# Kernel tuning notes

Hardware: AMD Instinct MI355X
Metric: run time of the kernel (lower is better)

## Reference

```python
import jax, jax.numpy as jnp
import numpy as np

NODE_DIM = 256
HID = 128        # out_channels per head
HEADS = 4
NLAYERS = 2
OUT_DIM = 128
LM, LT = 30, 50
N = LM + LT       # 80 nodes per duplex graph
F = HID * HEADS   # 512
B = 1024
LN_EPS = 1e-5

def _build_edges():
    off = LM
    ms = np.arange(LM - 1); md = ms + 1
    ts = off + np.arange(LT - 1); td = ts + 1
    s1 = np.concatenate([ms, md, ts, td]); d1 = np.concatenate([md, ms, td, ts])
    ms2 = np.arange(LM - 2); md2 = ms2 + 2
    ts2 = off + np.arange(LT - 2); td2 = ts2 + 2
    s2 = np.concatenate([ms2, md2, ts2, td2]); d2 = np.concatenate([md2, ms2, td2, ts2])
    src = np.concatenate([s1, s2]).astype(np.int32)
    dst = np.concatenate([d1, d2]).astype(np.int32)
    etype = np.concatenate([np.zeros(len(s1), np.int32), np.full(len(s2), 2, np.int32)])
    return src, dst, etype

_SRC0, _DST0, _ETYPE0 = _build_edges()
E0 = len(_SRC0)                      # 308 real edges (backbone + proximity)
SRC = jnp.concatenate([jnp.asarray(_SRC0), jnp.arange(N, dtype=jnp.int32)])  # + self loops
DST = jnp.concatenate([jnp.asarray(_DST0), jnp.arange(N, dtype=jnp.int32)])
DST_BASE = jnp.asarray(_DST0)
ETYPE = jnp.asarray(_ETYPE0)

def _ln(x, g, b):
    mu = x.mean(-1, keepdims=True)
    var = ((x - mu) ** 2).mean(-1, keepdims=True)
    return (x - mu) * jax.lax.rsqrt(var + LN_EPS) * g + b

def setup_inputs() -> dict:
    key = jax.random.key(0)
    ks = jax.random.split(key, 24)
    r = lambda k, shape, fan: jax.random.normal(k, shape, jnp.float32) / np.sqrt(fan)
    inp = {
        'mirna_enc': jax.random.normal(ks[0], (B, LM, NODE_DIM), jnp.float32),
        'target_enc': jax.random.normal(ks[1], (B, LT, NODE_DIM), jnp.float32),
        'node_type_emb': r(ks[2], (2, NODE_DIM), NODE_DIM),
        'edge_type_emb': r(ks[3], (3, HEADS), HEADS),
        'in_W': r(ks[4], (NODE_DIM, F), NODE_DIM), 'in_b': jnp.zeros((F,)),
        'in_ln_g': jnp.ones((F,)), 'in_ln_b': jnp.zeros((F,)),
        'gat_Wl': r(ks[5], (NLAYERS, F, F), F), 'gat_bl': jnp.zeros((NLAYERS, F)),
        'gat_Wr': r(ks[6], (NLAYERS, F, F), F), 'gat_br': jnp.zeros((NLAYERS, F)),
        'gat_We': r(ks[7], (NLAYERS, HEADS, F), HEADS),
        'gat_att': r(ks[8], (NLAYERS, HEADS, HID), HID),
        'gat_bo': jnp.zeros((NLAYERS, F)),
        'ln_g': jnp.ones((NLAYERS, F)), 'ln_b': jnp.zeros((NLAYERS, F)),
        'out_W': r(ks[9], (2 * F, OUT_DIM), 2 * F), 'out_b': jnp.zeros((OUT_DIM,)),
        'out_ln_g': jnp.ones((OUT_DIM,)), 'out_ln_b': jnp.zeros((OUT_DIM,)),
    }
    return inp

def reference(mirna_enc, target_enc, node_type_emb, edge_type_emb, in_W, in_b,
              in_ln_g, in_ln_b, gat_Wl, gat_bl, gat_Wr, gat_br, gat_We, gat_att,
              gat_bo, ln_g, ln_b, out_W, out_b, out_ln_g, out_ln_b):
    bsz = mirna_enc.shape[0]
    x = jnp.concatenate([mirna_enc + node_type_emb[0], target_enc + node_type_emb[1]], axis=1)  # [B,N,256]
    x = jax.nn.gelu(_ln(x @ in_W + in_b, in_ln_g, in_ln_b), approximate=False)  # [B,N,F]
    # edge attributes; self-loop attr = per-dst mean of incoming edge attrs (PyG fill_value='mean')
    base = edge_type_emb[ETYPE]  # [E0, HEADS]
    cnt = jax.ops.segment_sum(jnp.ones((E0, 1), base.dtype), DST_BASE, num_segments=N)
    sl = jax.ops.segment_sum(base, DST_BASE, num_segments=N) / jnp.maximum(cnt, 1.0)
    e_attr = jnp.concatenate([base, sl], axis=0)  # [E, HEADS]
    for i in range(NLAYERS):
        ee = (e_attr @ gat_We[i]).reshape(-1, HEADS, HID)                 # [E,H,C]
        xl = (x @ gat_Wl[i] + gat_bl[i]).reshape(bsz, N, HEADS, HID)
        xr = (x @ gat_Wr[i] + gat_br[i]).reshape(bsz, N, HEADS, HID)
        att_i = gat_att[i]
        def one_graph(xl_b, xr_b):
            msg = xl_b[SRC] + xr_b[DST] + ee                              # [E,H,C]
            a = jnp.einsum('ehc,hc->eh', jax.nn.leaky_relu(msg, 0.2), att_i)
            amax = jax.ops.segment_max(a, DST, num_segments=N)            # every node has a self loop
            ex = jnp.exp(a - amax[DST])
            den = jax.ops.segment_sum(ex, DST, num_segments=N)
            alpha = ex / den[DST]                                         # [E,H]
            out = jax.ops.segment_sum(alpha[:, :, None] * xl_b[SRC], DST, num_segments=N)
            return out.reshape(N, F)
        h = jax.vmap(one_graph)(xl, xr) + gat_bo[i]
        x = _ln(h + x, ln_g[i], ln_b[i])
        if i < NLAYERS - 1:
            x = jax.nn.gelu(x, approximate=False)
    pooled = jnp.concatenate([x.mean(axis=1), x.max(axis=1)], axis=-1)    # [B, 2F]
    return jax.nn.gelu(_ln(pooled @ out_W + out_b, out_ln_g, out_ln_b), approximate=False)
```

## Files before the change

kernel.cpp:

```cpp
#include <hip/hip_runtime.h>
#include <hip/hip_bf16.h>

typedef unsigned short u16;
typedef unsigned int u32;
typedef __attribute__((ext_vector_type(8))) short bf16x8;
typedef __attribute__((ext_vector_type(4))) float f32x4;

#define NB   1024
#define LMI  30
#define LTG  50
#define NN   80
#define ROWS (NB*NN)
#define FF   512
#define HH   4
#define CC   128

__device__ __forceinline__ u16 f2b(float f) {
    u32 u = __float_as_uint(f);
    u32 r = (u + 0x7FFFu + ((u >> 16) & 1u)) >> 16;
    return (u16)r;
}
__device__ __forceinline__ float b2f(u16 h) {
    return __uint_as_float(((u32)h) << 16);
}
__device__ __forceinline__ float gelu_f(float v) {
    return 0.5f * v * (1.0f + erff(v * 0.70710678118654752440f));
}
__device__ __forceinline__ void gload_lds16(const void* g, void* l) {
    __builtin_amdgcn_global_load_lds(
        (__attribute__((address_space(1))) void*)(uintptr_t)g,
        (__attribute__((address_space(3))) void*)(uintptr_t)l,
        16, 0, 0);
}

#define X_OFF     0ULL
#define XLR_OFF   83886080ULL
#define INWT_OFF  251658240ULL
#define WLRT_OFF  (INWT_OFF + 262144ULL)
#define BIAS_OFF  (WLRT_OFF + 2097152ULL)
#define EER_OFF   (BIAS_OFF + 8192ULL)
#define EES_OFF   (EER_OFF + 8192ULL)

__global__ __launch_bounds__(256)
void prep_misc(const float* __restrict__ in_W, const float* __restrict__ gat_Wl,
               const float* __restrict__ gat_bl, const float* __restrict__ gat_Wr,
               const float* __restrict__ gat_br, const float* __restrict__ gat_We,
               const float* __restrict__ eemb,
               u16* __restrict__ inWt, u16* __restrict__ Wlrt,
               float* __restrict__ biaslr, float* __restrict__ eereal,
               float* __restrict__ eeself)
{
    int idx = blockIdx.x * 256 + threadIdx.x;
    if (idx < 131072) {
        int n = idx >> 8, k = idx & 255;
        inWt[idx] = f2b(in_W[k * 512 + n]);
        return;
    }
    idx -= 131072;
    if (idx < 1048576) {
        int l = idx >> 19; int r = idx & 524287; int n = r >> 9, k = r & 511;
        float v = (n < 512) ? gat_Wl[(size_t)l * 262144 + (size_t)k * 512 + n]
                            : gat_Wr[(size_t)l * 262144 + (size_t)k * 512 + (n - 512)];
        Wlrt[idx] = f2b(v);
        return;
    }
    idx -= 1048576;
    if (idx < 2048) {
        int l = idx >> 10, n = idx & 1023;
        biaslr[idx] = (n < 512) ? gat_bl[l * 512 + n] : gat_br[l * 512 + (n - 512)];
        return;
    }
    idx -= 2048;
    if (idx < 2048) {
        int l = idx >> 10; int r = idx & 1023; int t = r >> 9, f = r & 511;
        int et = t ? 2 : 0;
        float v = 0.f;
        #pragma unroll
        for (int h = 0; h < 4; ++h)
            v += eemb[et * 4 + h] * gat_We[l * 2048 + h * 512 + f];
        eereal[idx] = v;
        return;
    }
    idx -= 2048;
    if (idx < 81920) {
        int l = idx / 40960; int r = idx % 40960; int n = r >> 9, f = r & 511;
        int LL = (n < LMI) ? LMI : LTG;
        int p  = (n < LMI) ? n : (n - LMI);
        float c1 = (float)((p >= 1) + (p <= LL - 2));
        float c2 = (float)((p >= 2) + (p <= LL - 3));
        float ic = 1.0f / (c1 + c2);
        float v = 0.f;
        #pragma unroll
        for (int h = 0; h < 4; ++h) {
            float attr = (c1 * eemb[0 * 4 + h] + c2 * eemb[2 * 4 + h]) * ic;
            v += attr * gat_We[l * 2048 + h * 512 + f];
        }
        eeself[idx] = v;
        return;
    }
}

__global__ __launch_bounds__(64)
void prep_xin(const float* __restrict__ mirna, const float* __restrict__ target,
              const float* __restrict__ nte, u16* __restrict__ xin)
{
    int bid = blockIdx.x;
    int b = bid / NN, n = bid % NN;
    int t = threadIdx.x;
    const float* src; const float* tv;
    if (n < LMI) { src = mirna + ((size_t)b * LMI + n) * 256; tv = nte; }
    else         { src = target + ((size_t)b * LTG + (n - LMI)) * 256; tv = nte + 256; }
    float4 v = *(const float4*)(src + t * 4);
    float4 e = *(const float4*)(tv + t * 4);
    u32 p0 = (u32)f2b(v.x + e.x) | ((u32)f2b(v.y + e.y) << 16);
    u32 p1 = (u32)f2b(v.z + e.z) | ((u32)f2b(v.w + e.w) << 16);
    *(uint2*)(xin + (size_t)bid * 256 + t * 4) = make_uint2(p0, p1);
}

template<int N, int K>
__global__ __launch_bounds__(512, 2)
void gemm_nt_bias(const u16* __restrict__ A, const u16* __restrict__ Bt,
                  const float* __restrict__ bias, u16* __restrict__ Cout)
{
    __shared__ __align__(16) u16 sm[4][2][8192];
    const int tid = threadIdx.x;
    const int w = tid >> 6, l = tid & 63;
    constexpr int ncb = N / 256;

    const int per = gridDim.x >> 3;
    const int nid = (blockIdx.x & 7) * per + (blockIdx.x >> 3);
    const int row0 = (nid / ncb) * 256;
    const int col0 = (nid % ncb) * 256;
    const int wr = w >> 2, wc = w & 3;

    const int srow = l >> 2;
    const int kperm = ((l & 3) ^ ((l >> 3) & 3)) * 8;
    const u16* Ag0 = A  + (size_t)(row0 +       w * 16 + srow) * K + kperm;
    const u16* Ag1 = A  + (size_t)(row0 + 128 + w * 16 + srow) * K + kperm;
    const u16* Bg0 = Bt + (size_t)(col0 +       w * 16 + srow) * K + kperm;
    const u16* Bg1 = Bt + (size_t)(col0 + 128 + w * 16 + srow) * K + kperm;
    const int lc0 = w * 512, lc1 = (8 + w) * 512;

#define STAGE_A(buf, t) do { \
        gload_lds16(Ag0 + (size_t)(t) * 32, &sm[buf][0][lc0]); \
        gload_lds16(Ag1 + (size_t)(t) * 32, &sm[buf][0][lc1]); } while (0)
#define STAGE_B(buf, t) do { \
        gload_lds16(Bg0 + (size_t)(t) * 32, &sm[buf][1][lc0]); \
        gload_lds16(Bg1 + (size_t)(t) * 32, &sm[buf][1][lc1]); } while (0)

    f32x4 acc[8][4];
    #pragma unroll
    for (int r = 0; r < 8; ++r)
        #pragma unroll
        for (int f = 0; f < 4; ++f)
            acc[r][f] = (f32x4){0.f, 0.f, 0.f, 0.f};

    constexpr int nsteps = K >> 5;
    STAGE_A(0, 0); STAGE_B(0, 0);
    STAGE_A(1, 1); STAGE_B(1, 1);

    const int pslot = ((l >> 4) ^ (((l & 15) >> 1) & 3)) * 8;
    const int abase = wr * 8 * 512 + (l & 15) * 32 + pslot;
    const int bbase = wc * 4 * 512 + (l & 15) * 32 + pslot;

    #pragma unroll
    for (int t = 0; t < nsteps; ++t) {
        const int buf = t & 3;
        if (t + 1 < nsteps) {
            asm volatile("s_waitcnt vmcnt(4)" ::: "memory");
        } else {
            asm volatile("s_waitcnt vmcnt(0)" ::: "memory");
        }
        __builtin_amdgcn_s_barrier();
        asm volatile("" ::: "memory");

        bf16x8 bfr[4], af[4];
        #pragma unroll
        for (int fc = 0; fc < 4; ++fc)
            bfr[fc] = *(const bf16x8*)&sm[buf][1][bbase + fc * 512];
        #pragma unroll
        for (int fr = 0; fr < 4; ++fr)
            af[fr] = *(const bf16x8*)&sm[buf][0][abase + fr * 512];
        if (t + 2 < nsteps) STAGE_A((t + 2) & 3, t + 2);
        __builtin_amdgcn_s_setprio(1);
        #pragma unroll
        for (int fr = 0; fr < 4; ++fr)
            #pragma unroll
            for (int fc = 0; fc < 4; ++fc)
                acc[fr][fc] = __builtin_amdgcn_mfma_f32_16x16x32_bf16(bfr[fc], af[fr], acc[fr][fc], 0, 0, 0);
        __builtin_amdgcn_s_setprio(0);
        asm volatile("" ::: "memory");
        __builtin_amdgcn_s_barrier();
        asm volatile("" ::: "memory");

        #pragma unroll
        for (int fr = 0; fr < 4; ++fr)
            af[fr] = *(const bf16x8*)&sm[buf][0][abase + (4 + fr) * 512];
        if (t + 2 < nsteps) STAGE_B((t + 2) & 3, t + 2);
        __builtin_amdgcn_s_setprio(1);
        #pragma unroll
        for (int fr = 0; fr < 4; ++fr)
            #pragma unroll
            for (int fc = 0; fc < 4; ++fc)
                acc[4 + fr][fc] = __builtin_amdgcn_mfma_f32_16x16x32_bf16(bfr[fc], af[fr], acc[4 + fr][fc], 0, 0, 0);
        __builtin_amdgcn_s_setprio(0);
        asm volatile("" ::: "memory");
    }
#undef STAGE_A
#undef STAGE_B

    #pragma unroll
    for (int ar = 0; ar < 8; ++ar) {
        int grow = row0 + wr * 128 + ar * 16 + (l & 15);
        #pragma unroll
        for (int fc = 0; fc < 4; ++fc) {
            int n0 = col0 + wc * 64 + fc * 16 + (l >> 4) * 4;
            float4 bv = *(const float4*)(bias + n0);
            u32 lo = (u32)f2b(acc[ar][fc][0] + bv.x) | ((u32)f2b(acc[ar][fc][1] + bv.y) << 16);
            u32 hi = (u32)f2b(acc[ar][fc][2] + bv.z) | ((u32)f2b(acc[ar][fc][3] + bv.w) << 16);
            *(uint2*)&Cout[(size_t)grow * N + n0] = make_uint2(lo, hi);
        }
    }
}

__global__ __launch_bounds__(256)
void ln_gelu_rows(u16* __restrict__ x, const float* __restrict__ g, const float* __restrict__ b)
{
    int w = threadIdx.x >> 6, l = threadIdx.x & 63;
    size_t row = (size_t)blockIdx.x * 4 + w;
    u16* rp = x + row * FF + l * 8;
    bf16x8 v = *(const bf16x8*)rp;
    float y[8]; float s = 0.f, q = 0.f;
    #pragma unroll
    for (int j = 0; j < 8; ++j) { y[j] = b2f((u16)v[j]); s += y[j]; q += y[j] * y[j]; }
    #pragma unroll
    for (int st = 32; st; st >>= 1) { s += __shfl_xor(s, st, 64); q += __shfl_xor(q, st, 64); }
    float mu = s * (1.0f / 512.0f);
    float var = q * (1.0f / 512.0f) - mu * mu;
    float rs = rsqrtf(var + 1e-5f);
    float4 g0 = *(const float4*)(g + l * 8), g1 = *(const float4*)(g + l * 8 + 4);
    float4 b0 = *(const float4*)(b + l * 8), b1 = *(const float4*)(b + l * 8 + 4);
    float gv[8] = {g0.x, g0.y, g0.z, g0.w, g1.x, g1.y, g1.z, g1.w};
    float bv[8] = {b0.x, b0.y, b0.z, b0.w, b1.x, b1.y, b1.z, b1.w};
    bf16x8 o;
    #pragma unroll
    for (int j = 0; j < 8; ++j) {
        float z = (y[j] - mu) * rs * gv[j] + bv[j];
        o[j] = (short)f2b(gelu_f(z));
    }
    *(bf16x8*)rp = o;
}

__global__ __launch_bounds__(256)
void gat_layer(u16* __restrict__ x, const u16* __restrict__ xlr,
               const float* __restrict__ att, const float* __restrict__ eereal,
               const float* __restrict__ eeself, const float* __restrict__ bo,
               const float* __restrict__ g, const float* __restrict__ bta,
               int apply_gelu)
{
    int tid = threadIdx.x;
    int h = tid >> 6, l = tid & 63;
    int s = l >> 4, t = l & 15;
    int row = blockIdx.x * 4 + s;
    int n = row % NN;
    int lo = (n < LMI) ? 0 : LMI;
    int hi = (n < LMI) ? (LMI - 1) : (NN - 1);
    int c = h * CC + t * 8;

    bf16x8 xrv = *(const bf16x8*)(xlr + (size_t)row * 1024 + 512 + c);
    float xr[8], atv[8];
    #pragma unroll
    for (int j = 0; j < 8; ++j) xr[j] = b2f((u16)xrv[j]);
    {
        float4 a0 = *(const float4*)(att + c), a1 = *(const float4*)(att + c + 4);
        atv[0]=a0.x; atv[1]=a0.y; atv[2]=a0.z; atv[3]=a0.w;
        atv[4]=a1.x; atv[5]=a1.y; atv[6]=a1.z; atv[7]=a1.w;
    }

    bf16x8 vsave[5];
    float p5[5];
    float amax = -1e30f;
    #pragma unroll
    for (int i = 0; i < 5; ++i) {
        int d = i - 2;
        int src = n + d;
        bool ok = (src >= lo) && (src <= hi);
        int dd = ok ? d : 0;
        bf16x8 vv = *(const bf16x8*)(xlr + (size_t)(row + dd) * 1024 + c);
        vsave[i] = vv;
        const float* ee = (i == 2) ? (eeself + (size_t)n * 512 + c)
                        : ((i == 1 || i == 3) ? (eereal + c) : (eereal + 512 + c));
        float4 e0 = *(const float4*)ee, e1 = *(const float4*)(ee + 4);
        float eez[8] = {e0.x, e0.y, e0.z, e0.w, e1.x, e1.y, e1.z, e1.w};
        float p = 0.f;
        #pragma unroll
        for (int j = 0; j < 8; ++j) {
            float m = b2f((u16)vv[j]) + xr[j] + eez[j];
            m = m > 0.f ? m : 0.2f * m;
            p += m * atv[j];
        }
        p += __shfl_xor(p, 1, 64);
        p += __shfl_xor(p, 2, 64);
        p += __shfl_xor(p, 4, 64);
        p += __shfl_xor(p, 8, 64);
        p = ok ? p : -1e30f;
        p5[i] = p;
        amax = fmaxf(amax, p);
    }
    float den = 0.f;
    float o[8] = {0.f,0.f,0.f,0.f,0.f,0.f,0.f,0.f};
    #pragma unroll
    for (int i = 0; i < 5; ++i) {
        float ex = __expf(p5[i] - amax);
        den += ex;
        #pragma unroll
        for (int j = 0; j < 8; ++j) o[j] += ex * b2f((u16)vsave[i][j]);
    }
    float inv = 1.0f / den;

    u16* xrow = x + (size_t)row * FF + c;
    bf16x8 xv = *(const bf16x8*)xrow;
    float bov[8];
    {
        float4 b0 = *(const float4*)(bo + c), b1 = *(const float4*)(bo + c + 4);
        bov[0]=b0.x; bov[1]=b0.y; bov[2]=b0.z; bov[3]=b0.w;
        bov[4]=b1.x; bov[5]=b1.y; bov[6]=b1.z; bov[7]=b1.w;
    }
    float y[8]; float sum = 0.f, sq = 0.f;
    #pragma unroll
    for (int j = 0; j < 8; ++j) {
        y[j] = o[j] * inv + bov[j] + b2f((u16)xv[j]);
        sum += y[j]; sq += y[j] * y[j];
    }
    sum += __shfl_xor(sum, 1, 64); sq += __shfl_xor(sq, 1, 64);
    sum += __shfl_xor(sum, 2, 64); sq += __shfl_xor(sq, 2, 64);
    sum += __shfl_xor(sum, 4, 64); sq += __shfl_xor(sq, 4, 64);
    sum += __shfl_xor(sum, 8, 64); sq += __shfl_xor(sq, 8, 64);

    __shared__ float ssum[4][4], ssq[4][4];
    if (t == 0) { ssum[h][s] = sum; ssq[h][s] = sq; }
    __syncthreads();
    float tot = ssum[0][s] + ssum[1][s] + ssum[2][s] + ssum[3][s];
    float tq  = ssq[0][s] + ssq[1][s] + ssq[2][s] + ssq[3][s];
    float mu = tot * (1.0f / 512.0f);
    float var = tq * (1.0f / 512.0f) - mu * mu;
    float rs = rsqrtf(var + 1e-5f);

    float gv[8], btv[8];
    {
        float4 g0 = *(const float4*)(g + c), g1 = *(const float4*)(g + c + 4);
        float4 t0 = *(const float4*)(bta + c), t1 = *(const float4*)(bta + c + 4);
        gv[0]=g0.x; gv[1]=g0.y; gv[2]=g0.z; gv[3]=g0.w;
        gv[4]=g1.x; gv[5]=g1.y; gv[6]=g1.z; gv[7]=g1.w;
        btv[0]=t0.x; btv[1]=t0.y; btv[2]=t0.z; btv[3]=t0.w;
        btv[4]=t1.x; btv[5]=t1.y; btv[6]=t1.z; btv[7]=t1.w;
    }
    bf16x8 ov;
    #pragma unroll
    for (int j = 0; j < 8; ++j) {
        float z = (y[j] - mu) * rs * gv[j] + btv[j];
        if (apply_gelu) z = gelu_f(z);
        ov[j] = (short)f2b(z);
    }
    *(bf16x8*)xrow = ov;
}

__global__ __launch_bounds__(512)
void pool_kernel(const u16* __restrict__ x, u16* __restrict__ pooled)
{
    int b = blockIdx.x;
    int f = threadIdx.x;
    const u16* base = x + (size_t)b * NN * FF + f;
    float s = 0.f, mx = -1e30f;
    #pragma unroll 4
    for (int n = 0; n < NN; ++n) {
        float v = b2f(base[(size_t)n * FF]);
        s += v; mx = fmaxf(mx, v);
    }
    pooled[(size_t)b * 1024 + f]       = f2b(s * (1.0f / 80.0f));
    pooled[(size_t)b * 1024 + 512 + f] = f2b(mx);
}

__global__ __launch_bounds__(128)
void out_head(const u16* __restrict__ pooled, const float* __restrict__ W,
              const float* __restrict__ bia, const float* __restrict__ g,
              const float* __restrict__ bt, float* __restrict__ out)
{
    int b = blockIdx.x;
    int j = threadIdx.x;
    __shared__ float prow[1024];
    for (int i = j; i < 1024; i += 128) prow[i] = b2f(pooled[(size_t)b * 1024 + i]);
    __syncthreads();
    float acc = 0.f;
    #pragma unroll 8
    for (int k = 0; k < 1024; ++k) acc += prow[k] * W[k * 128 + j];
    acc += bia[j];
    float s = acc, q = acc * acc;
    #pragma unroll
    for (int st = 32; st; st >>= 1) { s += __shfl_xor(s, st, 64); q += __shfl_xor(q, st, 64); }
    __shared__ float ps[2], pq[2];
    int w = j >> 6;
    if ((j & 63) == 0) { ps[w] = s; pq[w] = q; }
    __syncthreads();
    float tot = ps[0] + ps[1], tq = pq[0] + pq[1];
    float mu = tot * (1.0f / 128.0f);
    float var = tq * (1.0f / 128.0f) - mu * mu;
    float rs = rsqrtf(var + 1e-5f);
    float z = (acc - mu) * rs * g[j] + bt[j];
    out[(size_t)b * 128 + j] = gelu_f(z);
}

extern "C" void kernel_launch(void* const* d_in, const int* in_sizes, int n_in,
                              void* d_out, int out_size, void* d_ws, size_t ws_size,
                              hipStream_t stream)
{
    (void)in_sizes; (void)n_in; (void)out_size; (void)ws_size;
    const float* mirna    = (const float*)d_in[0];
    const float* target   = (const float*)d_in[1];
    const float* nte      = (const float*)d_in[2];
    const float* eemb     = (const float*)d_in[3];
    const float* in_W     = (const float*)d_in[4];
    const float* in_b     = (const float*)d_in[5];
    const float* in_ln_g  = (const float*)d_in[6];
    const float* in_ln_b  = (const float*)d_in[7];
    const float* gat_Wl   = (const float*)d_in[8];
    const float* gat_bl   = (const float*)d_in[9];
    const float* gat_Wr   = (const float*)d_in[10];
    const float* gat_br   = (const float*)d_in[11];
    const float* gat_We   = (const float*)d_in[12];
    const float* gat_att  = (const float*)d_in[13];
    const float* gat_bo   = (const float*)d_in[14];
    const float* ln_g     = (const float*)d_in[15];
    const float* ln_b     = (const float*)d_in[16];
    const float* out_W    = (const float*)d_in[17];
    const float* out_b    = (const float*)d_in[18];
    const float* out_ln_g = (const float*)d_in[19];
    const float* out_ln_b = (const float*)d_in[20];

    char* ws = (char*)d_ws;
    u16*   x      = (u16*)(ws + X_OFF);
    u16*   xlr    = (u16*)(ws + XLR_OFF);
    u16*   xin    = xlr;
    u16*   pooled = xlr;
    u16*   inWt   = (u16*)(ws + INWT_OFF);
    u16*   Wlrt   = (u16*)(ws + WLRT_OFF);
    float* biaslr = (float*)(ws + BIAS_OFF);
    float* eereal = (float*)(ws + EER_OFF);
    float* eeself = (float*)(ws + EES_OFF);

    prep_misc<<<4944, 256, 0, stream>>>(in_W, gat_Wl, gat_bl, gat_Wr, gat_br, gat_We, eemb,
                                        inWt, Wlrt, biaslr, eereal, eeself);
    prep_xin<<<ROWS, 64, 0, stream>>>(mirna, target, nte, xin);

    gemm_nt_bias<512, 256><<<(ROWS / 256) * 2, 512, 0, stream>>>(xin, inWt, in_b, x);
    ln_gelu_rows<<<ROWS / 4, 256, 0, stream>>>(x, in_ln_g, in_ln_b);

    for (int l = 0; l < 2; ++l) {
        gemm_nt_bias<1024, 512><<<(ROWS / 256) * 4, 512, 0, stream>>>(
            x, Wlrt + (size_t)l * 524288, biaslr + l * 1024, xlr);
        gat_layer<<<ROWS / 4, 256, 0, stream>>>(x, xlr,
                                                gat_att + l * 512,
                                                eereal + l * 1024,
                                                eeself + (size_t)l * 40960,
                                                gat_bo + l * 512,
                                                ln_g + l * 512, ln_b + l * 512,
                                                (l == 0) ? 1 : 0);
    }

    pool_kernel<<<NB, 512, 0, stream>>>(x, pooled);
    out_head<<<NB, 128, 0, stream>>>(pooled, out_W, out_b, out_ln_g, out_ln_b, (float*)d_out);
}
```

Measured before the change: 565.9 us.

## Restructure GEMM mainloop to double-buffered K=64 tiles with quadrant-split MFMA phases

Switches the bf16 GEMM from a 4-deep ring of K=32 stages to a 2-buffer scheme with K=64 tiles, using a new XOR swizzle for the LDS layout. Each iteration now waits for all outstanding loads, issues the next tile's prefetch, and computes the 256x256 output in four quadrant phases separated by barriers. The aim is fewer loop iterations and barriers per unit of K and larger global loads per stage. The cost is a full vmcnt(0) wait each iteration, which shortens the prefetch distance, plus several extra barriers. The new register fragment layout also changes register pressure.

```diff
diff --git a/kernel.cpp b/kernel.cpp
--- a/kernel.cpp
+++ b/kernel.cpp
@@ -122,10 +122,11 @@
 void gemm_nt_bias(const u16* __restrict__ A, const u16* __restrict__ Bt,
                   const float* __restrict__ bias, u16* __restrict__ Cout)
 {
-    __shared__ __align__(16) u16 sm[4][2][8192];
+    __shared__ __align__(16) u16 sm[2][2][16384];
     const int tid = threadIdx.x;
     const int w = tid >> 6, l = tid & 63;
     constexpr int ncb = N / 256;
+    constexpr int KT = K / 64;
 
     const int per = gridDim.x >> 3;
     const int nid = (blockIdx.x & 7) * per + (blockIdx.x >> 3);
@@ -133,20 +134,24 @@
     const int col0 = (nid % ncb) * 256;
     const int wr = w >> 2, wc = w & 3;
 
-    const int srow = l >> 2;
-    const int kperm = ((l & 3) ^ ((l >> 3) & 3)) * 8;
-    const u16* Ag0 = A  + (size_t)(row0 +       w * 16 + srow) * K + kperm;
-    const u16* Ag1 = A  + (size_t)(row0 + 128 + w * 16 + srow) * K + kperm;
-    const u16* Bg0 = Bt + (size_t)(col0 +       w * 16 + srow) * K + kperm;
-    const u16* Bg1 = Bt + (size_t)(col0 + 128 + w * 16 + srow) * K + kperm;
-    const int lc0 = w * 512, lc1 = (8 + w) * 512;
-
-#define STAGE_A(buf, t) do { \
-        gload_lds16(Ag0 + (size_t)(t) * 32, &sm[buf][0][lc0]); \
-        gload_lds16(Ag1 + (size_t)(t) * 32, &sm[buf][0][lc1]); } while (0)
-#define STAGE_B(buf, t) do { \
-        gload_lds16(Bg0 + (size_t)(t) * 32, &sm[buf][1][lc0]); \
-        gload_lds16(Bg1 + (size_t)(t) * 32, &sm[buf][1][lc1]); } while (0)
+    const int srow = w * 8 + (l >> 3);
+    const int sks  = ((l & 7) ^ (l >> 3)) * 8;
+    const u16* Abase = A  + (size_t)(row0 + srow) * K + sks;
+    const u16* Bbase = Bt + (size_t)(col0 + srow) * K + sks;
+    const int ldst = w * 512;
+
+#define STAGE_KT(buf, kt) do {                                          \
+        const u16* _a = Abase + (size_t)(kt) * 64;                      \
+        const u16* _b = Bbase + (size_t)(kt) * 64;                      \
+        gload_lds16(_a,                   &sm[buf][0][ldst]);           \
+        gload_lds16(_a + (size_t)64  * K, &sm[buf][0][4096  + ldst]);   \
+        gload_lds16(_a + (size_t)128 * K, &sm[buf][0][8192  + ldst]);   \
+        gload_lds16(_a + (size_t)192 * K, &sm[buf][0][12288 + ldst]);   \
+        gload_lds16(_b,                   &sm[buf][1][ldst]);           \
+        gload_lds16(_b + (size_t)64  * K, &sm[buf][1][4096  + ldst]);   \
+        gload_lds16(_b + (size_t)128 * K, &sm[buf][1][8192  + ldst]);   \
+        gload_lds16(_b + (size_t)192 * K, &sm[buf][1][12288 + ldst]);   \
+    } while (0)
 
     f32x4 acc[8][4];
     #pragma unroll
@@ -155,66 +160,96 @@
         for (int f = 0; f < 4; ++f)
             acc[r][f] = (f32x4){0.f, 0.f, 0.f, 0.f};
 
-    constexpr int nsteps = K >> 5;
-    STAGE_A(0, 0); STAGE_B(0, 0);
-    STAGE_A(1, 1); STAGE_B(1, 1);
-
-    const int pslot = ((l >> 4) ^ (((l & 15) >> 1) & 3)) * 8;
-    const int abase = wr * 8 * 512 + (l & 15) * 32 + pslot;
-    const int bbase = wc * 4 * 512 + (l & 15) * 32 + pslot;
-
-    #pragma unroll
-    for (int t = 0; t < nsteps; ++t) {
-        const int buf = t & 3;
-        if (t + 1 < nsteps) {
-            asm volatile("s_waitcnt vmcnt(4)" ::: "memory");
-        } else {
-            asm volatile("s_waitcnt vmcnt(0)" ::: "memory");
-        }
-        __builtin_amdgcn_s_barrier();
-        asm volatile("" ::: "memory");
-
-        bf16x8 bfr[4], af[4];
-        #pragma unroll
-        for (int fc = 0; fc < 4; ++fc)
-            bfr[fc] = *(const bf16x8*)&sm[buf][1][bbase + fc * 512];
-        #pragma unroll
-        for (int fr = 0; fr < 4; ++fr)
-            af[fr] = *(const bf16x8*)&sm[buf][0][abase + fr * 512];
-        if (t + 2 < nsteps) STAGE_A((t + 2) & 3, t + 2);
+    const int ll = l & 15, lh = l >> 4;
+    const int x0 = ((lh)     ^ (ll & 7)) * 8;
+    const int x1 = ((4 + lh) ^ (ll & 7)) * 8;
+    const int aB = wr * 8192 + ll * 64;
+    const int bB = (wc >> 1) * 8192 + ((wc & 1) * 64 + ll) * 64;
+
+    STAGE_KT(0, 0);
+
+    #pragma unroll
+    for (int kt = 0; kt < KT; ++kt) {
+        const int cur = kt & 1;
+        asm volatile("s_waitcnt vmcnt(0)" ::: "memory");
+        __builtin_amdgcn_s_barrier();
+
+        bf16x8 a0[4][2], a1[4][2], b0[2][2], b1[2][2];
+        #pragma unroll
+        for (int fr = 0; fr < 4; ++fr) {
+            a0[fr][0] = *(const bf16x8*)&sm[cur][0][aB + fr * 1024 + x0];
+            a0[fr][1] = *(const bf16x8*)&sm[cur][0][aB + fr * 1024 + x1];
+        }
+        #pragma unroll
+        for (int fc = 0; fc < 2; ++fc) {
+            b0[fc][0] = *(const bf16x8*)&sm[cur][1][bB + fc * 1024 + x0];
+            b0[fc][1] = *(const bf16x8*)&sm[cur][1][bB + fc * 1024 + x1];
+        }
+        if (kt + 1 < KT) STAGE_KT(cur ^ 1, kt + 1);
+        __builtin_amdgcn_s_barrier();
         __builtin_amdgcn_s_setprio(1);
         #pragma unroll
         for (int fr = 0; fr < 4; ++fr)
             #pragma unroll
-            for (int fc = 0; fc < 4; ++fc)
-                acc[fr][fc] = __builtin_amdgcn_mfma_f32_16x16x32_bf16(bfr[fc], af[fr], acc[fr][fc], 0, 0, 0);
+            for (int fc = 0; fc < 2; ++fc)
+                #pragma unroll
+                for (int kk = 0; kk < 2; ++kk)
+                    acc[fr][fc] = __builtin_amdgcn_mfma_f32_16x16x32_bf16(b0[fc][kk], a0[fr][kk], acc[fr][fc], 0, 0, 0);
         __builtin_amdgcn_s_setprio(0);
-        asm volatile("" ::: "memory");
-        __builtin_amdgcn_s_barrier();
-        asm volatile("" ::: "memory");
-
-        #pragma unroll
-        for (int fr = 0; fr < 4; ++fr)
-            af[fr] = *(const bf16x8*)&sm[buf][0][abase + (4 + fr) * 512];
-        if (t + 2 < nsteps) STAGE_B((t + 2) & 3, t + 2);
+        __builtin_amdgcn_s_barrier();
+
+        #pragma unroll
+        for (int fc = 0; fc < 2; ++fc) {
+            b1[fc][0] = *(const bf16x8*)&sm[cur][1][bB + (2 + fc) * 1024 + x0];
+            b1[fc][1] = *(const bf16x8*)&sm[cur][1][bB + (2 + fc) * 1024 + x1];
+        }
+        __builtin_amdgcn_s_barrier();
         __builtin_amdgcn_s_setprio(1);
         #pragma unroll
         for (int fr = 0; fr < 4; ++fr)
             #pragma unroll
-            for (int fc = 0; fc < 4; ++fc)
-                acc[4 + fr][fc] = __builtin_amdgcn_mfma_f32_16x16x32_bf16(bfr[fc], af[fr], acc[4 + fr][fc], 0, 0, 0);
+            for (int fc = 0; fc < 2; ++fc)
+                #pragma unroll
+                for (int kk = 0; kk < 2; ++kk)
+                    acc[fr][2 + fc] = __builtin_amdgcn_mfma_f32_16x16x32_bf16(b1[fc][kk], a0[fr][kk], acc[fr][2 + fc], 0, 0, 0);
         __builtin_amdgcn_s_setprio(0);
-        asm volatile("" ::: "memory");
-    }
-#undef STAGE_A
-#undef STAGE_B
+        __builtin_amdgcn_s_barrier();
+
+        #pragma unroll
+        for (int fr = 0; fr < 4; ++fr) {
+            a1[fr][0] = *(const bf16x8*)&sm[cur][0][aB + (4 + fr) * 1024 + x0];
+            a1[fr][1] = *(const bf16x8*)&sm[cur][0][aB + (4 + fr) * 1024 + x1];
+        }
+        __builtin_amdgcn_s_barrier();
+        __builtin_amdgcn_s_setprio(1);
+        #pragma unroll
+        for (int fr = 0; fr < 4; ++fr)
+            #pragma unroll
+            for (int fc = 0; fc < 2; ++fc)
+                #pragma unroll
+                for (int kk = 0; kk < 2; ++kk)
+                    acc[4 + fr][fc] = __builtin_amdgcn_mfma_f32_16x16x32_bf16(b0[fc][kk], a1[fr][kk], acc[4 + fr][fc], 0, 0, 0);
+        __builtin_amdgcn_s_setprio(0);
+        __builtin_amdgcn_s_barrier();
+
+        __builtin_amdgcn_s_setprio(1);
+        #pragma unroll
+        for (int fr = 0; fr < 4; ++fr)
+            #pragma unroll
+            for (int fc = 0; fc < 2; ++fc)
+                #pragma unroll
+                for (int kk = 0; kk < 2; ++kk)
+                    acc[4 + fr][2 + fc] = __builtin_amdgcn_mfma_f32_16x16x32_bf16(b1[fc][kk], a1[fr][kk], acc[4 + fr][2 + fc], 0, 0, 0);
+        __builtin_amdgcn_s_setprio(0);
+    }
+#undef STAGE_KT
 
     #pragma unroll
     for (int ar = 0; ar < 8; ++ar) {
-        int grow = row0 + wr * 128 + ar * 16 + (l & 15);
+        int grow = row0 + wr * 128 + ar * 16 + ll;
         #pragma unroll
         for (int fc = 0; fc < 4; ++fc) {
-            int n0 = col0 + wc * 64 + fc * 16 + (l >> 4) * 4;
+            int n0 = col0 + wc * 64 + fc * 16 + lh * 4;
             float4 bv = *(const float4*)(bias + n0);
             u32 lo = (u32)f2b(acc[ar][fc][0] + bv.x) | ((u32)f2b(acc[ar][fc][1] + bv.y) << 16);
             u32 hi = (u32)f2b(acc[ar][fc][2] + bv.z) | ((u32)f2b(acc[ar][fc][3] + bv.w) << 16);
```

New measurement: 573.5 us. No clear change (+1.3%).
